# Optimization experiments

Measured on AMD Instinct MI355X. Metric: run time of the kernel, lower is better.

Reference implementation:

```python
import jax, jax.numpy as jnp
import numpy as np

NUM_EXPERTS = 8
HIDDEN = 1024
INTER = 1024
TOKENS = 2048
TOPK = 2


def setup_inputs() -> dict:
    key = jax.random.key(0)
    ks = jax.random.split(key, 7)
    hidden_states = jax.random.normal(ks[0], (TOKENS, HIDDEN), dtype=jnp.float32)
    router_weights = jax.random.uniform(ks[1], (TOKENS, TOPK), dtype=jnp.float32)
    selected_experts = jax.random.randint(ks[2], (TOKENS, TOPK), 0, NUM_EXPERTS, dtype=jnp.int32)
    token_per_expert = jax.random.randint(ks[3], (NUM_EXPERTS,), 0, 512, dtype=jnp.int32)
    # torch Linear weight layout is [out, in]; chunked along out-dim into E experts.
    # gate/up: [E, INTER, HIDDEN]; down: [E, HIDDEN, INTER]
    scale_h = 1.0 / np.sqrt(HIDDEN)
    scale_i = 1.0 / np.sqrt(INTER)
    gate_w = jax.random.normal(ks[4], (NUM_EXPERTS, INTER, HIDDEN), dtype=jnp.float32) * scale_h
    up_w = jax.random.normal(ks[5], (NUM_EXPERTS, INTER, HIDDEN), dtype=jnp.float32) * scale_h
    down_w = jax.random.normal(ks[6], (NUM_EXPERTS, HIDDEN, INTER), dtype=jnp.float32) * scale_i
    return {
        "hidden_states": hidden_states,
        "router_weights": router_weights,
        "selected_experts": selected_experts,
        "token_per_expert": token_per_expert,
        "gate_w": gate_w,
        "up_w": up_w,
        "down_w": down_w,
    }


def reference(hidden_states, router_weights, selected_experts, token_per_expert, gate_w, up_w, down_w):
    # Math equivalent of permute -> grouped GEMM (gate/up SwiGLU, down) -> unpermute+weighted combine.
    # Each (token, k) pair is routed to expert selected_experts[t,k] and scaled by router_weights[t,k]
    # (cast to fp32 as in the original), then summed over k.
    # Grouped GEMM out = x @ W_e^T; we evaluate every expert densely over all tokens and
    # combine with a one-hot routing matrix (clean, fully vectorized reference).
    x = hidden_states  # [T, H]
    g = jnp.einsum('th,eih->eti', x, gate_w)          # [E, T, I]
    u = jnp.einsum('th,eih->eti', x, up_w)            # [E, T, I]
    h = jax.nn.silu(g) * u                            # [E, T, I]
    out_e = jnp.einsum('eti,ehi->eth', h, down_w)     # [E, T, H]
    # combine[t, e] = sum_k router_weights[t, k] * 1[selected_experts[t, k] == e]
    onehot = jax.nn.one_hot(selected_experts, NUM_EXPERTS, dtype=jnp.float32)  # [T, K, E]
    combine = jnp.einsum('tk,tke->te', router_weights.astype(jnp.float32), onehot)  # [T, E]
    y = jnp.einsum('te,eth->th', combine, out_e)      # [T, H]
    return y
```

## Files before the change

kernel.cpp:

```cpp
#include <hip/hip_runtime.h>

#define HID   1024
#define NEXP  8
#define NPAIR 4096
#define BMPAD 128
#define PERM_MAX (NPAIR + NEXP * BMPAD)
#define MT_MAX (PERM_MAX / 128)

typedef unsigned short u16;
typedef __attribute__((ext_vector_type(8))) short bf16x8;
typedef __attribute__((ext_vector_type(4))) float f32x4;
typedef __attribute__((ext_vector_type(4))) unsigned short us4;

static __device__ __forceinline__ u16 f2bf(float f) {
  union { float f; unsigned u; } v; v.f = f;
  unsigned u = v.u;
  unsigned r = (u + 0x7fffu + ((u >> 16) & 1u)) >> 16;
  return (u16)r;
}

static __device__ __forceinline__ void gload16(const void* g, void* l) {
  __builtin_amdgcn_global_load_lds(
      (const __attribute__((address_space(1))) unsigned int*)g,
      (__attribute__((address_space(3))) unsigned int*)l, 16, 0, 0);
}

static __device__ __forceinline__ f32x4 mfma_bf16(bf16x8 a, bf16x8 b, f32x4 c) {
  return __builtin_amdgcn_mfma_f32_16x16x32_bf16(a, b, c, 0, 0, 0);
}

__global__ __launch_bounds__(256) void k_prep(const float* __restrict__ x,
                                              u16* __restrict__ xb,
                                              float* __restrict__ out) {
  int i = blockIdx.x * 256 + threadIdx.x;
  int base = i * 8;
  f32x4 v0 = *(const f32x4*)(x + base);
  f32x4 v1 = *(const f32x4*)(x + base + 4);
  us4 a = { f2bf(v0[0]), f2bf(v0[1]), f2bf(v0[2]), f2bf(v0[3]) };
  us4 b = { f2bf(v1[0]), f2bf(v1[1]), f2bf(v1[2]), f2bf(v1[3]) };
  *(us4*)(xb + base)     = a;
  *(us4*)(xb + base + 4) = b;
  f32x4 z = {0.f, 0.f, 0.f, 0.f};
  *(f32x4*)(out + base)     = z;
  *(f32x4*)(out + base + 4) = z;
}

__global__ __launch_bounds__(256) void k_convw(const float* __restrict__ g,
                                               const float* __restrict__ u,
                                               const float* __restrict__ d,
                                               u16* __restrict__ gb,
                                               u16* __restrict__ ub,
                                               u16* __restrict__ db) {
  const long NTH = 3L << 20;
  for (long i = (long)blockIdx.x * 256 + threadIdx.x; i < NTH; i += (long)gridDim.x * 256) {
    int which = (int)(i >> 20);
    long off = (i & ((1L << 20) - 1)) * 8;
    const float* src = which == 0 ? g : (which == 1 ? u : d);
    u16* dst = which == 0 ? gb : (which == 1 ? ub : db);
    f32x4 v0 = *(const f32x4*)(src + off);
    f32x4 v1 = *(const f32x4*)(src + off + 4);
    us4 a = { f2bf(v0[0]), f2bf(v0[1]), f2bf(v0[2]), f2bf(v0[3]) };
    us4 b = { f2bf(v1[0]), f2bf(v1[1]), f2bf(v1[2]), f2bf(v1[3]) };
    *(us4*)(dst + off)     = a;
    *(us4*)(dst + off + 4) = b;
  }
}

__global__ __launch_bounds__(256) void k_route(const int* __restrict__ sel,
                                               int* __restrict__ hdr,
                                               int* __restrict__ perm) {
  __shared__ int cnt[NEXP];
  __shared__ int cur[NEXP];
  int tid = threadIdx.x;
  if (tid < NEXP) cnt[tid] = 0;
  __syncthreads();
  for (int p = tid; p < NPAIR; p += 256) atomicAdd(&cnt[sel[p]], 1);
  __syncthreads();
  if (tid == 0) {
    int acc = 0;
    for (int e = 0; e < NEXP; e++) {
      hdr[e] = acc;
      cur[e] = acc;
      acc += (cnt[e] + 127) & ~127;
    }
    hdr[NEXP] = acc;
  }
  __syncthreads();
  for (int i = tid; i < PERM_MAX; i += 256) perm[i] = -1;
  __syncthreads();
  for (int p = tid; p < NPAIR; p += 256) {
    int e = sel[p];
    int slot = atomicAdd(&cur[e], 1);
    perm[slot] = p;
  }
}

__global__ __launch_bounds__(256) void k_gateup(const u16* __restrict__ xb,
                                                const u16* __restrict__ gwb,
                                                const u16* __restrict__ uwb,
                                                const int* __restrict__ hdr,
                                                const int* __restrict__ perm,
                                                u16* __restrict__ hbuf) {
  __shared__ __align__(16) u16 lA[128 * 64];
  __shared__ __align__(16) u16 lBg[64 * 64];
  __shared__ __align__(16) u16 lBu[64 * 64];

  const int tid = threadIdx.x, lane = tid & 63, wv = tid >> 6;
  const int n0 = blockIdx.x * 64, m0 = blockIdx.y * 128;
  const int total = hdr[NEXP];
  if (m0 >= total) return;
  int e = 0;
  #pragma unroll
  for (int k = 1; k < NEXP; k++) if (m0 >= hdr[k]) e = k;

  const u16* srcA[4]; u16* dstA[4];
  #pragma unroll
  for (int j = 0; j < 4; j++) {
    int rt = wv * 32 + j * 8 + (lane >> 3);
    int p = perm[m0 + rt];
    int tok = (p < 0) ? 0 : (p >> 1);
    int sw = (lane & 7) ^ (rt & 7);
    srcA[j] = xb + (size_t)tok * HID + sw * 8;
    dstA[j] = &lA[(wv * 32 + j * 8) * 64];
  }
  const u16* srcG[2]; const u16* srcU[2]; int dstBo[2];
  const size_t eb = (size_t)e * (1 << 20);
  #pragma unroll
  for (int j = 0; j < 2; j++) {
    int rt = wv * 16 + j * 8 + (lane >> 3);
    int sw = (lane & 7) ^ (rt & 7);
    srcG[j] = gwb + eb + (size_t)(n0 + rt) * HID + sw * 8;
    srcU[j] = uwb + eb + (size_t)(n0 + rt) * HID + sw * 8;
    dstBo[j] = (wv * 16 + j * 8) * 64;
  }

  const int wm = wv >> 1, wn = wv & 1;
  const int fr = lane & 15, fq = lane >> 4;

  f32x4 accg[4][2], accu[4][2];
  #pragma unroll
  for (int a = 0; a < 4; a++)
    #pragma unroll
    for (int b = 0; b < 2; b++) {
      accg[a][b] = (f32x4){0.f, 0.f, 0.f, 0.f};
      accu[a][b] = (f32x4){0.f, 0.f, 0.f, 0.f};
    }

  for (int kk = 0; kk < HID / 64; kk++) {
    const int k0 = kk * 64;
    #pragma unroll
    for (int j = 0; j < 4; j++) gload16(srcA[j] + k0, dstA[j]);
    #pragma unroll
    for (int j = 0; j < 2; j++) {
      gload16(srcG[j] + k0, &lBg[dstBo[j]]);
      gload16(srcU[j] + k0, &lBu[dstBo[j]]);
    }
    __syncthreads();
    #pragma unroll
    for (int kk2 = 0; kk2 < 2; kk2++) {
      bf16x8 af[4], bg[2], bu[2];
      #pragma unroll
      for (int m2 = 0; m2 < 4; m2++) {
        int r = wm * 64 + m2 * 16 + fr, q = kk2 * 4 + fq;
        af[m2] = *(const bf16x8*)&lA[r * 64 + (q ^ (r & 7)) * 8];
      }
      #pragma unroll
      for (int n2 = 0; n2 < 2; n2++) {
        int r = wn * 32 + n2 * 16 + fr, q = kk2 * 4 + fq;
        bg[n2] = *(const bf16x8*)&lBg[r * 64 + (q ^ (r & 7)) * 8];
        bu[n2] = *(const bf16x8*)&lBu[r * 64 + (q ^ (r & 7)) * 8];
      }
      #pragma unroll
      for (int m2 = 0; m2 < 4; m2++)
        #pragma unroll
        for (int n2 = 0; n2 < 2; n2++) {
          accg[m2][n2] = mfma_bf16(af[m2], bg[n2], accg[m2][n2]);
          accu[m2][n2] = mfma_bf16(af[m2], bu[n2], accu[m2][n2]);
        }
    }
    __syncthreads();
  }

  #pragma unroll
  for (int m2 = 0; m2 < 4; m2++)
    #pragma unroll
    for (int n2 = 0; n2 < 2; n2++)
      #pragma unroll
      for (int q = 0; q < 4; q++) {
        int row = m0 + wm * 64 + m2 * 16 + fq * 4 + q;
        int col = n0 + wn * 32 + n2 * 16 + fr;
        float g = accg[m2][n2][q];
        float u = accu[m2][n2][q];
        float h = (g / (1.0f + __expf(-g))) * u;
        hbuf[(size_t)row * HID + col] = f2bf(h);
      }
}

__global__ __launch_bounds__(256) void k_down(const u16* __restrict__ hbuf,
                                              const u16* __restrict__ dwb,
                                              const int* __restrict__ hdr,
                                              const int* __restrict__ perm,
                                              const float* __restrict__ rw,
                                              float* __restrict__ out) {
  __shared__ __align__(16) u16 lA[128 * 64];
  __shared__ __align__(16) u16 lB[64 * 64];

  const int tid = threadIdx.x, lane = tid & 63, wv = tid >> 6;
  const int n0 = blockIdx.x * 64, m0 = blockIdx.y * 128;
  const int total = hdr[NEXP];
  if (m0 >= total) return;
  int e = 0;
  #pragma unroll
  for (int k = 1; k < NEXP; k++) if (m0 >= hdr[k]) e = k;

  const u16* srcA[4]; u16* dstA[4];
  #pragma unroll
  for (int j = 0; j < 4; j++) {
    int rt = wv * 32 + j * 8 + (lane >> 3);
    int sw = (lane & 7) ^ (rt & 7);
    srcA[j] = hbuf + (size_t)(m0 + rt) * HID + sw * 8;
    dstA[j] = &lA[(wv * 32 + j * 8) * 64];
  }
  const u16* srcB[2]; int dstBo[2];
  const size_t eb = (size_t)e * (1 << 20);
  #pragma unroll
  for (int j = 0; j < 2; j++) {
    int rt = wv * 16 + j * 8 + (lane >> 3);
    int sw = (lane & 7) ^ (rt & 7);
    srcB[j] = dwb + eb + (size_t)(n0 + rt) * HID + sw * 8;
    dstBo[j] = (wv * 16 + j * 8) * 64;
  }

  const int wm = wv >> 1, wn = wv & 1;
  const int fr = lane & 15, fq = lane >> 4;

  f32x4 acc[4][2];
  #pragma unroll
  for (int a = 0; a < 4; a++)
    #pragma unroll
    for (int b = 0; b < 2; b++) acc[a][b] = (f32x4){0.f, 0.f, 0.f, 0.f};

  for (int kk = 0; kk < HID / 64; kk++) {
    const int k0 = kk * 64;
    #pragma unroll
    for (int j = 0; j < 4; j++) gload16(srcA[j] + k0, dstA[j]);
    #pragma unroll
    for (int j = 0; j < 2; j++) gload16(srcB[j] + k0, &lB[dstBo[j]]);
    __syncthreads();
    #pragma unroll
    for (int kk2 = 0; kk2 < 2; kk2++) {
      bf16x8 af[4], bf[2];
      #pragma unroll
      for (int m2 = 0; m2 < 4; m2++) {
        int r = wm * 64 + m2 * 16 + fr, q = kk2 * 4 + fq;
        af[m2] = *(const bf16x8*)&lA[r * 64 + (q ^ (r & 7)) * 8];
      }
      #pragma unroll
      for (int n2 = 0; n2 < 2; n2++) {
        int r = wn * 32 + n2 * 16 + fr, q = kk2 * 4 + fq;
        bf[n2] = *(const bf16x8*)&lB[r * 64 + (q ^ (r & 7)) * 8];
      }
      #pragma unroll
      for (int m2 = 0; m2 < 4; m2++)
        #pragma unroll
        for (int n2 = 0; n2 < 2; n2++)
          acc[m2][n2] = mfma_bf16(af[m2], bf[n2], acc[m2][n2]);
    }
    __syncthreads();
  }

  #pragma unroll
  for (int m2 = 0; m2 < 4; m2++)
    #pragma unroll
    for (int q = 0; q < 4; q++) {
      int row = m0 + wm * 64 + m2 * 16 + fq * 4 + q;
      int p = perm[row];
      if (p < 0) continue;
      int t = p >> 1;
      float w = rw[p];
      #pragma unroll
      for (int n2 = 0; n2 < 2; n2++) {
        int col = n0 + wn * 32 + n2 * 16 + fr;
        atomicAdd(&out[(size_t)t * HID + col], acc[m2][n2][q] * w);
      }
    }
}

extern "C" void kernel_launch(void* const* d_in, const int* in_sizes, int n_in,
                              void* d_out, int out_size, void* d_ws, size_t ws_size,
                              hipStream_t stream) {
  const float* x   = (const float*)d_in[0];
  const float* rw  = (const float*)d_in[1];
  const int*   sel = (const int*)d_in[2];
  const float* gw  = (const float*)d_in[4];
  const float* uw  = (const float*)d_in[5];
  const float* dw  = (const float*)d_in[6];
  float* out = (float*)d_out;

  char* ws = (char*)d_ws;
  int*  hdr  = (int*)ws;
  int*  perm = (int*)(ws + 1024);
  u16*  xb   = (u16*)(ws + (1 << 16));
  u16*  gwb  = xb + (2 << 20);
  u16*  uwb  = gwb + (8 << 20);
  u16*  dwb  = uwb + (8 << 20);
  u16*  hbuf = dwb + (8 << 20);

  k_prep <<<dim3(1024), dim3(256), 0, stream>>>(x, xb, out);
  k_convw<<<dim3(4096), dim3(256), 0, stream>>>(gw, uw, dw, gwb, uwb, dwb);
  k_route<<<dim3(1),    dim3(256), 0, stream>>>(sel, hdr, perm);
  k_gateup<<<dim3(16, MT_MAX), dim3(256), 0, stream>>>(xb, gwb, uwb, hdr, perm, hbuf);
  k_down  <<<dim3(16, MT_MAX), dim3(256), 0, stream>>>(hbuf, dwb, hdr, perm, rw, out);
}
```

Baseline: 114.4 us.

## Fuse fp32-to-bf16 weight conversion into GEMM loads with double-buffered LDS

Drops the separate weight-conversion kernel. The gate/up and down GEMMs now read fp32 weights directly into registers, pack them to bf16 and write them into LDS themselves. LDS tiles are double-buffered so the next K-slice's loads overlap the current MFMA work. This removes a full read and write of 48MB of fp32 weights plus bf16 copies and one launch. The cost is that each weight tile is re-read and re-converted by every M-tile block (up to 40 per expert column), doubling fp32 weight bytes per block and adding register pressure and more LDS.

```diff
diff --git a/kernel.cpp b/kernel.cpp
--- a/kernel.cpp
+++ b/kernel.cpp
@@ -1,4 +1,5 @@
 #include <hip/hip_runtime.h>
+#include <hip/hip_bf16.h>
 
 #define HID   1024
 #define NEXP  8
@@ -11,12 +12,18 @@
 typedef __attribute__((ext_vector_type(8))) short bf16x8;
 typedef __attribute__((ext_vector_type(4))) float f32x4;
 typedef __attribute__((ext_vector_type(4))) unsigned short us4;
+typedef __attribute__((ext_vector_type(4))) unsigned int u32x4;
 
 static __device__ __forceinline__ u16 f2bf(float f) {
   union { float f; unsigned u; } v; v.f = f;
   unsigned u = v.u;
   unsigned r = (u + 0x7fffu + ((u >> 16) & 1u)) >> 16;
   return (u16)r;
+}
+
+static __device__ __forceinline__ unsigned pk2(float a, float b) {
+  __hip_bfloat162 h = __float22bfloat162_rn(make_float2(a, b));
+  union { __hip_bfloat162 h; unsigned u; } c; c.h = h; return c.u;
 }
 
 static __device__ __forceinline__ void gload16(const void* g, void* l) {
@@ -45,27 +52,6 @@
   *(f32x4*)(out + base + 4) = z;
 }
 
-__global__ __launch_bounds__(256) void k_convw(const float* __restrict__ g,
-                                               const float* __restrict__ u,
-                                               const float* __restrict__ d,
-                                               u16* __restrict__ gb,
-                                               u16* __restrict__ ub,
-                                               u16* __restrict__ db) {
-  const long NTH = 3L << 20;
-  for (long i = (long)blockIdx.x * 256 + threadIdx.x; i < NTH; i += (long)gridDim.x * 256) {
-    int which = (int)(i >> 20);
-    long off = (i & ((1L << 20) - 1)) * 8;
-    const float* src = which == 0 ? g : (which == 1 ? u : d);
-    u16* dst = which == 0 ? gb : (which == 1 ? ub : db);
-    f32x4 v0 = *(const f32x4*)(src + off);
-    f32x4 v1 = *(const f32x4*)(src + off + 4);
-    us4 a = { f2bf(v0[0]), f2bf(v0[1]), f2bf(v0[2]), f2bf(v0[3]) };
-    us4 b = { f2bf(v1[0]), f2bf(v1[1]), f2bf(v1[2]), f2bf(v1[3]) };
-    *(us4*)(dst + off)     = a;
-    *(us4*)(dst + off + 4) = b;
-  }
-}
-
 __global__ __launch_bounds__(256) void k_route(const int* __restrict__ sel,
                                                int* __restrict__ hdr,
                                                int* __restrict__ perm) {
@@ -96,24 +82,23 @@
 }
 
 __global__ __launch_bounds__(256) void k_gateup(const u16* __restrict__ xb,
-                                                const u16* __restrict__ gwb,
-                                                const u16* __restrict__ uwb,
+                                                const float* __restrict__ gw,
+                                                const float* __restrict__ uw,
                                                 const int* __restrict__ hdr,
                                                 const int* __restrict__ perm,
                                                 u16* __restrict__ hbuf) {
-  __shared__ __align__(16) u16 lA[128 * 64];
-  __shared__ __align__(16) u16 lBg[64 * 64];
-  __shared__ __align__(16) u16 lBu[64 * 64];
+  __shared__ __align__(16) u16 lA[2][128 * 64];
+  __shared__ __align__(16) u16 lBg[2][64 * 64];
+  __shared__ __align__(16) u16 lBu[2][64 * 64];
 
   const int tid = threadIdx.x, lane = tid & 63, wv = tid >> 6;
   const int n0 = blockIdx.x * 64, m0 = blockIdx.y * 128;
-  const int total = hdr[NEXP];
-  if (m0 >= total) return;
+  if (m0 >= hdr[NEXP]) return;
   int e = 0;
   #pragma unroll
   for (int k = 1; k < NEXP; k++) if (m0 >= hdr[k]) e = k;
 
-  const u16* srcA[4]; u16* dstA[4];
+  const u16* srcA[4]; int dstAo[4];
   #pragma unroll
   for (int j = 0; j < 4; j++) {
     int rt = wv * 32 + j * 8 + (lane >> 3);
@@ -121,22 +106,20 @@
     int tok = (p < 0) ? 0 : (p >> 1);
     int sw = (lane & 7) ^ (rt & 7);
     srcA[j] = xb + (size_t)tok * HID + sw * 8;
-    dstA[j] = &lA[(wv * 32 + j * 8) * 64];
-  }
-  const u16* srcG[2]; const u16* srcU[2]; int dstBo[2];
+    dstAo[j] = (wv * 32 + j * 8) * 64;
+  }
+  const int br = wv * 16 + (lane >> 2);
+  const int cb = (lane & 3) * 16;
   const size_t eb = (size_t)e * (1 << 20);
-  #pragma unroll
-  for (int j = 0; j < 2; j++) {
-    int rt = wv * 16 + j * 8 + (lane >> 3);
-    int sw = (lane & 7) ^ (rt & 7);
-    srcG[j] = gwb + eb + (size_t)(n0 + rt) * HID + sw * 8;
-    srcU[j] = uwb + eb + (size_t)(n0 + rt) * HID + sw * 8;
-    dstBo[j] = (wv * 16 + j * 8) * 64;
-  }
+  const float* pG = gw + eb + (size_t)(n0 + br) * HID + cb;
+  const float* pU = uw + eb + (size_t)(n0 + br) * HID + cb;
+  const int bws0 = br * 64 + ((((lane & 3) * 2 + 0) ^ (br & 7)) * 8);
+  const int bws1 = br * 64 + ((((lane & 3) * 2 + 1) ^ (br & 7)) * 8);
 
   const int wm = wv >> 1, wn = wv & 1;
   const int fr = lane & 15, fq = lane >> 4;
 
+  f32x4 vg[4], vu[4];
   f32x4 accg[4][2], accu[4][2];
   #pragma unroll
   for (int a = 0; a < 4; a++)
@@ -146,40 +129,63 @@
       accu[a][b] = (f32x4){0.f, 0.f, 0.f, 0.f};
     }
 
-  for (int kk = 0; kk < HID / 64; kk++) {
-    const int k0 = kk * 64;
-    #pragma unroll
-    for (int j = 0; j < 4; j++) gload16(srcA[j] + k0, dstA[j]);
-    #pragma unroll
-    for (int j = 0; j < 2; j++) {
-      gload16(srcG[j] + k0, &lBg[dstBo[j]]);
-      gload16(srcU[j] + k0, &lBu[dstBo[j]]);
-    }
+#define GU_ISSUE(B, K0) { const int k0_ = (K0);                                   \
+    _Pragma("unroll") for (int j = 0; j < 4; j++)                                 \
+      gload16(srcA[j] + k0_, &lA[B][dstAo[j]]);                                   \
+    _Pragma("unroll") for (int i = 0; i < 4; i++) {                               \
+      vg[i] = *(const f32x4*)(pG + k0_ + i * 4);                                  \
+      vu[i] = *(const f32x4*)(pU + k0_ + i * 4);                                  \
+    } }
+
+#define GU_CVTW(B) {                                                              \
+    u32x4 w0 = { pk2(vg[0][0], vg[0][1]), pk2(vg[0][2], vg[0][3]),                \
+                 pk2(vg[1][0], vg[1][1]), pk2(vg[1][2], vg[1][3]) };              \
+    *(u32x4*)&lBg[B][bws0] = w0;                                                  \
+    u32x4 w1 = { pk2(vg[2][0], vg[2][1]), pk2(vg[2][2], vg[2][3]),                \
+                 pk2(vg[3][0], vg[3][1]), pk2(vg[3][2], vg[3][3]) };              \
+    *(u32x4*)&lBg[B][bws1] = w1;                                                  \
+    u32x4 w2 = { pk2(vu[0][0], vu[0][1]), pk2(vu[0][2], vu[0][3]),                \
+                 pk2(vu[1][0], vu[1][1]), pk2(vu[1][2], vu[1][3]) };              \
+    *(u32x4*)&lBu[B][bws0] = w2;                                                  \
+    u32x4 w3 = { pk2(vu[2][0], vu[2][1]), pk2(vu[2][2], vu[2][3]),                \
+                 pk2(vu[3][0], vu[3][1]), pk2(vu[3][2], vu[3][3]) };              \
+    *(u32x4*)&lBu[B][bws1] = w3; }
+
+#define GU_COMP(B) {                                                              \
+    _Pragma("unroll") for (int kk2 = 0; kk2 < 2; kk2++) {                         \
+      bf16x8 af[4], bg[2], bu[2];                                                 \
+      _Pragma("unroll") for (int m2 = 0; m2 < 4; m2++) {                          \
+        int r = wm * 64 + m2 * 16 + fr, q = kk2 * 4 + fq;                         \
+        af[m2] = *(const bf16x8*)&lA[B][r * 64 + (q ^ (r & 7)) * 8];              \
+      }                                                                           \
+      _Pragma("unroll") for (int n2 = 0; n2 < 2; n2++) {                          \
+        int r = wn * 32 + n2 * 16 + fr, q = kk2 * 4 + fq;                         \
+        bg[n2] = *(const bf16x8*)&lBg[B][r * 64 + (q ^ (r & 7)) * 8];             \
+        bu[n2] = *(const bf16x8*)&lBu[B][r * 64 + (q ^ (r & 7)) * 8];             \
+      }                                                                           \
+      _Pragma("unroll") for (int m2 = 0; m2 < 4; m2++)                            \
+        _Pragma("unroll") for (int n2 = 0; n2 < 2; n2++) {                        \
+          accg[m2][n2] = mfma_bf16(af[m2], bg[n2], accg[m2][n2]);                 \
+          accu[m2][n2] = mfma_bf16(af[m2], bu[n2], accu[m2][n2]);                 \
+        }                                                                         \
+    } }
+
+  GU_ISSUE(0, 0);
+  GU_CVTW(0);
+  __syncthreads();
+  for (int kk = 0; kk < 16; kk += 2) {
+    GU_ISSUE(1, (kk + 1) * 64);
+    GU_COMP(0);
+    GU_CVTW(1);
     __syncthreads();
-    #pragma unroll
-    for (int kk2 = 0; kk2 < 2; kk2++) {
-      bf16x8 af[4], bg[2], bu[2];
-      #pragma unroll
-      for (int m2 = 0; m2 < 4; m2++) {
-        int r = wm * 64 + m2 * 16 + fr, q = kk2 * 4 + fq;
-        af[m2] = *(const bf16x8*)&lA[r * 64 + (q ^ (r & 7)) * 8];
-      }
-      #pragma unroll
-      for (int n2 = 0; n2 < 2; n2++) {
-        int r = wn * 32 + n2 * 16 + fr, q = kk2 * 4 + fq;
-        bg[n2] = *(const bf16x8*)&lBg[r * 64 + (q ^ (r & 7)) * 8];
-        bu[n2] = *(const bf16x8*)&lBu[r * 64 + (q ^ (r & 7)) * 8];
-      }
-      #pragma unroll
-      for (int m2 = 0; m2 < 4; m2++)
-        #pragma unroll
-        for (int n2 = 0; n2 < 2; n2++) {
-          accg[m2][n2] = mfma_bf16(af[m2], bg[n2], accg[m2][n2]);
-          accu[m2][n2] = mfma_bf16(af[m2], bu[n2], accu[m2][n2]);
-        }
-    }
+    if (kk + 2 < 16) { GU_ISSUE(0, (kk + 2) * 64); }
+    GU_COMP(1);
+    if (kk + 2 < 16) { GU_CVTW(0); }
     __syncthreads();
   }
+#undef GU_ISSUE
+#undef GU_CVTW
+#undef GU_COMP
 
   #pragma unroll
   for (int m2 = 0; m2 < 4; m2++)
@@ -197,77 +203,92 @@
 }
 
 __global__ __launch_bounds__(256) void k_down(const u16* __restrict__ hbuf,
-                                              const u16* __restrict__ dwb,
+                                              const float* __restrict__ dw,
                                               const int* __restrict__ hdr,
                                               const int* __restrict__ perm,
                                               const float* __restrict__ rw,
                                               float* __restrict__ out) {
-  __shared__ __align__(16) u16 lA[128 * 64];
-  __shared__ __align__(16) u16 lB[64 * 64];
+  __shared__ __align__(16) u16 lA[2][128 * 64];
+  __shared__ __align__(16) u16 lB[2][64 * 64];
 
   const int tid = threadIdx.x, lane = tid & 63, wv = tid >> 6;
   const int n0 = blockIdx.x * 64, m0 = blockIdx.y * 128;
-  const int total = hdr[NEXP];
-  if (m0 >= total) return;
+  if (m0 >= hdr[NEXP]) return;
   int e = 0;
   #pragma unroll
   for (int k = 1; k < NEXP; k++) if (m0 >= hdr[k]) e = k;
 
-  const u16* srcA[4]; u16* dstA[4];
+  const u16* srcA[4]; int dstAo[4];
   #pragma unroll
   for (int j = 0; j < 4; j++) {
     int rt = wv * 32 + j * 8 + (lane >> 3);
     int sw = (lane & 7) ^ (rt & 7);
     srcA[j] = hbuf + (size_t)(m0 + rt) * HID + sw * 8;
-    dstA[j] = &lA[(wv * 32 + j * 8) * 64];
-  }
-  const u16* srcB[2]; int dstBo[2];
+    dstAo[j] = (wv * 32 + j * 8) * 64;
+  }
+  const int br = wv * 16 + (lane >> 2);
+  const int cb = (lane & 3) * 16;
   const size_t eb = (size_t)e * (1 << 20);
-  #pragma unroll
-  for (int j = 0; j < 2; j++) {
-    int rt = wv * 16 + j * 8 + (lane >> 3);
-    int sw = (lane & 7) ^ (rt & 7);
-    srcB[j] = dwb + eb + (size_t)(n0 + rt) * HID + sw * 8;
-    dstBo[j] = (wv * 16 + j * 8) * 64;
-  }
+  const float* pB = dw + eb + (size_t)(n0 + br) * HID + cb;
+  const int bws0 = br * 64 + ((((lane & 3) * 2 + 0) ^ (br & 7)) * 8);
+  const int bws1 = br * 64 + ((((lane & 3) * 2 + 1) ^ (br & 7)) * 8);
 
   const int wm = wv >> 1, wn = wv & 1;
   const int fr = lane & 15, fq = lane >> 4;
 
+  f32x4 vb[4];
   f32x4 acc[4][2];
   #pragma unroll
   for (int a = 0; a < 4; a++)
     #pragma unroll
     for (int b = 0; b < 2; b++) acc[a][b] = (f32x4){0.f, 0.f, 0.f, 0.f};
 
-  for (int kk = 0; kk < HID / 64; kk++) {
-    const int k0 = kk * 64;
-    #pragma unroll
-    for (int j = 0; j < 4; j++) gload16(srcA[j] + k0, dstA[j]);
-    #pragma unroll
-    for (int j = 0; j < 2; j++) gload16(srcB[j] + k0, &lB[dstBo[j]]);
+#define DN_ISSUE(B, K0) { const int k0_ = (K0);                                   \
+    _Pragma("unroll") for (int j = 0; j < 4; j++)                                 \
+      gload16(srcA[j] + k0_, &lA[B][dstAo[j]]);                                   \
+    _Pragma("unroll") for (int i = 0; i < 4; i++)                                 \
+      vb[i] = *(const f32x4*)(pB + k0_ + i * 4); }
+
+#define DN_CVTW(B) {                                                              \
+    u32x4 w0 = { pk2(vb[0][0], vb[0][1]), pk2(vb[0][2], vb[0][3]),                \
+                 pk2(vb[1][0], vb[1][1]), pk2(vb[1][2], vb[1][3]) };              \
+    *(u32x4*)&lB[B][bws0] = w0;                                                   \
+    u32x4 w1 = { pk2(vb[2][0], vb[2][1]), pk2(vb[2][2], vb[2][3]),                \
+                 pk2(vb[3][0], vb[3][1]), pk2(vb[3][2], vb[3][3]) };              \
+    *(u32x4*)&lB[B][bws1] = w1; }
+
+#define DN_COMP(B) {                                                              \
+    _Pragma("unroll") for (int kk2 = 0; kk2 < 2; kk2++) {                         \
+      bf16x8 af[4], bf[2];                                                        \
+      _Pragma("unroll") for (int m2 = 0; m2 < 4; m2++) {                          \
+        int r = wm * 64 + m2 * 16 + fr, q = kk2 * 4 + fq;                         \
+        af[m2] = *(const bf16x8*)&lA[B][r * 64 + (q ^ (r & 7)) * 8];              \
+      }                                                                           \
+      _Pragma("unroll") for (int n2 = 0; n2 < 2; n2++) {                          \
+        int r = wn * 32 + n2 * 16 + fr, q = kk2 * 4 + fq;                         \
+        bf[n2] = *(const bf16x8*)&lB[B][r * 64 + (q ^ (r & 7)) * 8];              \
+      }                                                                           \
+      _Pragma("unroll") for (int m2 = 0; m2 < 4; m2++)                            \
+        _Pragma("unroll") for (int n2 = 0; n2 < 2; n2++)                          \
+          acc[m2][n2] = mfma_bf16(af[m2], bf[n2], acc[m2][n2]);                   \
+    } }
+
+  DN_ISSUE(0, 0);
+  DN_CVTW(0);
+  __syncthreads();
+  for (int kk = 0; kk < 16; kk += 2) {
+    DN_ISSUE(1, (kk + 1) * 64);
+    DN_COMP(0);
+    DN_CVTW(1);
     __syncthreads();
-    #pragma unroll
-    for (int kk2 = 0; kk2 < 2; kk2++) {
-      bf16x8 af[4], bf[2];
-      #pragma unroll
-      for (int m2 = 0; m2 < 4; m2++) {
-        int r = wm * 64 + m2 * 16 + fr, q = kk2 * 4 + fq;
-        af[m2] = *(const bf16x8*)&lA[r * 64 + (q ^ (r & 7)) * 8];
-      }
-      #pragma unroll
-      for (int n2 = 0; n2 < 2; n2++) {
-        int r = wn * 32 + n2 * 16 + fr, q = kk2 * 4 + fq;
-        bf[n2] = *(const bf16x8*)&lB[r * 64 + (q ^ (r & 7)) * 8];
-      }
-      #pragma unroll
-      for (int m2 = 0; m2 < 4; m2++)
-        #pragma unroll
-        for (int n2 = 0; n2 < 2; n2++)
-          acc[m2][n2] = mfma_bf16(af[m2], bf[n2], acc[m2][n2]);
-    }
+    if (kk + 2 < 16) { DN_ISSUE(0, (kk + 2) * 64); }
+    DN_COMP(1);
+    if (kk + 2 < 16) { DN_CVTW(0); }
     __syncthreads();
   }
+#undef DN_ISSUE
+#undef DN_CVTW
+#undef DN_COMP
 
   #pragma unroll
   for (int m2 = 0; m2 < 4; m2++)
@@ -301,14 +322,10 @@
   int*  hdr  = (int*)ws;
   int*  perm = (int*)(ws + 1024);
   u16*  xb   = (u16*)(ws + (1 << 16));
-  u16*  gwb  = xb + (2 << 20);
-  u16*  uwb  = gwb + (8 << 20);
-  u16*  dwb  = uwb + (8 << 20);
-  u16*  hbuf = dwb + (8 << 20);
+  u16*  hbuf = xb + (2 << 20);
 
   k_prep <<<dim3(1024), dim3(256), 0, stream>>>(x, xb, out);
-  k_convw<<<dim3(4096), dim3(256), 0, stream>>>(gw, uw, dw, gwb, uwb, dwb);
   k_route<<<dim3(1),    dim3(256), 0, stream>>>(sel, hdr, perm);
-  k_gateup<<<dim3(16, MT_MAX), dim3(256), 0, stream>>>(xb, gwb, uwb, hdr, perm, hbuf);
-  k_down  <<<dim3(16, MT_MAX), dim3(256), 0, stream>>>(hbuf, dwb, hdr, perm, rw, out);
-}
+  k_gateup<<<dim3(16, MT_MAX), dim3(256), 0, stream>>>(xb, gw, uw, hdr, perm, hbuf);
+  k_down  <<<dim3(16, MT_MAX), dim3(256), 0, stream>>>(hbuf, dw, hdr, perm, rw, out);
+}
```

Measured after the change: 115.3 us. No clear change (+0.8%).

## Fuse weight conversion into prep and gate-up kernels, use per-expert grids

Applied to the files above, without the earlier changes.

Gate/up weight conversion moves into the prep kernel, and the down-weight conversion is folded into the tail of the gate-up kernel, which removes the separate conversion launch. Both GEMM kernels now use a 1D grid indexed by expert, N tile and M tile, and loop over M tiles in strides of 16. This avoids launching blocks that exit early on padded M tiles. The gate-up N tile shrinks to 32 to get more blocks. The trade-offs are narrower gate-up tiles with less B-tile reuse per A load, and extra conversion work in the gate-up tail.

```diff
diff --git a/kernel.cpp b/kernel.cpp
--- a/kernel.cpp
+++ b/kernel.cpp
@@ -1,11 +1,11 @@
 #include <hip/hip_runtime.h>
+#include <hip/hip_bf16.h>
 
 #define HID   1024
 #define NEXP  8
 #define NPAIR 4096
-#define BMPAD 128
-#define PERM_MAX (NPAIR + NEXP * BMPAD)
-#define MT_MAX (PERM_MAX / 128)
+#define PERM_MAX (NPAIR + NEXP * 128)
+#define MT_CAP 16
 
 typedef unsigned short u16;
 typedef __attribute__((ext_vector_type(8))) short bf16x8;
@@ -29,40 +29,36 @@
   return __builtin_amdgcn_mfma_f32_16x16x32_bf16(a, b, c, 0, 0, 0);
 }
 
-__global__ __launch_bounds__(256) void k_prep(const float* __restrict__ x,
-                                              u16* __restrict__ xb,
-                                              float* __restrict__ out) {
-  int i = blockIdx.x * 256 + threadIdx.x;
-  int base = i * 8;
-  f32x4 v0 = *(const f32x4*)(x + base);
-  f32x4 v1 = *(const f32x4*)(x + base + 4);
+static __device__ __forceinline__ void conv8(const float* src, u16* dst) {
+  f32x4 v0 = *(const f32x4*)src;
+  f32x4 v1 = *(const f32x4*)(src + 4);
   us4 a = { f2bf(v0[0]), f2bf(v0[1]), f2bf(v0[2]), f2bf(v0[3]) };
   us4 b = { f2bf(v1[0]), f2bf(v1[1]), f2bf(v1[2]), f2bf(v1[3]) };
-  *(us4*)(xb + base)     = a;
-  *(us4*)(xb + base + 4) = b;
-  f32x4 z = {0.f, 0.f, 0.f, 0.f};
-  *(f32x4*)(out + base)     = z;
-  *(f32x4*)(out + base + 4) = z;
-}
-
-__global__ __launch_bounds__(256) void k_convw(const float* __restrict__ g,
-                                               const float* __restrict__ u,
-                                               const float* __restrict__ d,
-                                               u16* __restrict__ gb,
-                                               u16* __restrict__ ub,
-                                               u16* __restrict__ db) {
-  const long NTH = 3L << 20;
-  for (long i = (long)blockIdx.x * 256 + threadIdx.x; i < NTH; i += (long)gridDim.x * 256) {
-    int which = (int)(i >> 20);
-    long off = (i & ((1L << 20) - 1)) * 8;
-    const float* src = which == 0 ? g : (which == 1 ? u : d);
-    u16* dst = which == 0 ? gb : (which == 1 ? ub : db);
-    f32x4 v0 = *(const f32x4*)(src + off);
-    f32x4 v1 = *(const f32x4*)(src + off + 4);
-    us4 a = { f2bf(v0[0]), f2bf(v0[1]), f2bf(v0[2]), f2bf(v0[3]) };
-    us4 b = { f2bf(v1[0]), f2bf(v1[1]), f2bf(v1[2]), f2bf(v1[3]) };
-    *(us4*)(dst + off)     = a;
-    *(us4*)(dst + off + 4) = b;
+  *(us4*)dst       = a;
+  *(us4*)(dst + 4) = b;
+}
+
+__global__ __launch_bounds__(256) void k_prep(const float* __restrict__ x,
+                                              const float* __restrict__ gw,
+                                              const float* __restrict__ uw,
+                                              u16* __restrict__ xb,
+                                              u16* __restrict__ gwb,
+                                              u16* __restrict__ uwb,
+                                              float* __restrict__ out) {
+  const int i = blockIdx.x * 256 + threadIdx.x;
+  {
+    int base = i * 8;
+    conv8(x + base, xb + base);
+    f32x4 z = {0.f, 0.f, 0.f, 0.f};
+    *(f32x4*)(out + base)     = z;
+    *(f32x4*)(out + base + 4) = z;
+  }
+  #pragma unroll
+  for (int j = 0; j < 4; j++) {
+    long c = (long)i + 262144L * j;
+    long off = c * 8;
+    conv8(gw + off, gwb + off);
+    conv8(uw + off, uwb + off);
   }
 }
 
@@ -98,102 +94,100 @@
 __global__ __launch_bounds__(256) void k_gateup(const u16* __restrict__ xb,
                                                 const u16* __restrict__ gwb,
                                                 const u16* __restrict__ uwb,
+                                                const float* __restrict__ dw,
+                                                u16* __restrict__ dwb,
                                                 const int* __restrict__ hdr,
                                                 const int* __restrict__ perm,
                                                 u16* __restrict__ hbuf) {
   __shared__ __align__(16) u16 lA[128 * 64];
-  __shared__ __align__(16) u16 lBg[64 * 64];
-  __shared__ __align__(16) u16 lBu[64 * 64];
+  __shared__ __align__(16) u16 lBg[32 * 64];
+  __shared__ __align__(16) u16 lBu[32 * 64];
 
   const int tid = threadIdx.x, lane = tid & 63, wv = tid >> 6;
-  const int n0 = blockIdx.x * 64, m0 = blockIdx.y * 128;
-  const int total = hdr[NEXP];
-  if (m0 >= total) return;
-  int e = 0;
-  #pragma unroll
-  for (int k = 1; k < NEXP; k++) if (m0 >= hdr[k]) e = k;
-
-  const u16* srcA[4]; u16* dstA[4];
-  #pragma unroll
-  for (int j = 0; j < 4; j++) {
-    int rt = wv * 32 + j * 8 + (lane >> 3);
-    int p = perm[m0 + rt];
-    int tok = (p < 0) ? 0 : (p >> 1);
-    int sw = (lane & 7) ^ (rt & 7);
-    srcA[j] = xb + (size_t)tok * HID + sw * 8;
-    dstA[j] = &lA[(wv * 32 + j * 8) * 64];
-  }
-  const u16* srcG[2]; const u16* srcU[2]; int dstBo[2];
-  const size_t eb = (size_t)e * (1 << 20);
-  #pragma unroll
-  for (int j = 0; j < 2; j++) {
-    int rt = wv * 16 + j * 8 + (lane >> 3);
-    int sw = (lane & 7) ^ (rt & 7);
-    srcG[j] = gwb + eb + (size_t)(n0 + rt) * HID + sw * 8;
-    srcU[j] = uwb + eb + (size_t)(n0 + rt) * HID + sw * 8;
-    dstBo[j] = (wv * 16 + j * 8) * 64;
-  }
+  const int bid = blockIdx.x;
+  const int e = bid & 7;
+  const int idx = bid >> 3;
+  const int nt = idx >> 4;
+  const int mt0 = idx & 15;
+  const int seg0 = hdr[e];
+  const int mcnt = (hdr[e + 1] - seg0) >> 7;
+  const int n0 = nt * 32;
 
   const int wm = wv >> 1, wn = wv & 1;
   const int fr = lane & 15, fq = lane >> 4;
-
-  f32x4 accg[4][2], accu[4][2];
-  #pragma unroll
-  for (int a = 0; a < 4; a++)
-    #pragma unroll
-    for (int b = 0; b < 2; b++) {
-      accg[a][b] = (f32x4){0.f, 0.f, 0.f, 0.f};
-      accu[a][b] = (f32x4){0.f, 0.f, 0.f, 0.f};
-    }
-
-  for (int kk = 0; kk < HID / 64; kk++) {
-    const int k0 = kk * 64;
-    #pragma unroll
-    for (int j = 0; j < 4; j++) gload16(srcA[j] + k0, dstA[j]);
-    #pragma unroll
-    for (int j = 0; j < 2; j++) {
-      gload16(srcG[j] + k0, &lBg[dstBo[j]]);
-      gload16(srcU[j] + k0, &lBu[dstBo[j]]);
-    }
-    __syncthreads();
-    #pragma unroll
-    for (int kk2 = 0; kk2 < 2; kk2++) {
-      bf16x8 af[4], bg[2], bu[2];
-      #pragma unroll
-      for (int m2 = 0; m2 < 4; m2++) {
-        int r = wm * 64 + m2 * 16 + fr, q = kk2 * 4 + fq;
-        af[m2] = *(const bf16x8*)&lA[r * 64 + (q ^ (r & 7)) * 8];
+  const size_t eb = (size_t)e << 20;
+
+  const int br = tid >> 3, bq = tid & 7;
+  const u16* srcG = gwb + eb + (size_t)(n0 + br) * HID + (bq ^ (br & 7)) * 8;
+  const u16* srcU = uwb + eb + (size_t)(n0 + br) * HID + (bq ^ (br & 7)) * 8;
+  const int dstBo = br * 64 + bq * 8;
+
+  for (int mt = mt0; mt < mcnt; mt += MT_CAP) {
+    const int m0 = seg0 + mt * 128;
+    const u16* srcA[4]; int dstAo[4];
+    #pragma unroll
+    for (int j = 0; j < 4; j++) {
+      int c = tid + 256 * j;
+      int r = c >> 3, q = c & 7;
+      int p = perm[m0 + r];
+      int tok = (p < 0) ? 0 : (p >> 1);
+      srcA[j] = xb + (size_t)tok * HID + (q ^ (r & 7)) * 8;
+      dstAo[j] = r * 64 + q * 8;
+    }
+
+    f32x4 accg[4], accu[4];
+    #pragma unroll
+    for (int a = 0; a < 4; a++) {
+      accg[a] = (f32x4){0.f, 0.f, 0.f, 0.f};
+      accu[a] = (f32x4){0.f, 0.f, 0.f, 0.f};
+    }
+
+    for (int kk = 0; kk < 16; kk++) {
+      const int k0 = kk * 64;
+      #pragma unroll
+      for (int j = 0; j < 4; j++) gload16(srcA[j] + k0, &lA[dstAo[j]]);
+      gload16(srcG + k0, &lBg[dstBo]);
+      gload16(srcU + k0, &lBu[dstBo]);
+      __syncthreads();
+      #pragma unroll
+      for (int kk2 = 0; kk2 < 2; kk2++) {
+        bf16x8 af[4], bg, bu;
+        #pragma unroll
+        for (int m2 = 0; m2 < 4; m2++) {
+          int r = wm * 64 + m2 * 16 + fr, q = kk2 * 4 + fq;
+          af[m2] = *(const bf16x8*)&lA[r * 64 + (q ^ (r & 7)) * 8];
+        }
+        {
+          int r = wn * 16 + fr, q = kk2 * 4 + fq;
+          bg = *(const bf16x8*)&lBg[r * 64 + (q ^ (r & 7)) * 8];
+          bu = *(const bf16x8*)&lBu[r * 64 + (q ^ (r & 7)) * 8];
+        }
+        #pragma unroll
+        for (int m2 = 0; m2 < 4; m2++) {
+          accg[m2] = mfma_bf16(af[m2], bg, accg[m2]);
+          accu[m2] = mfma_bf16(af[m2], bu, accu[m2]);
+        }
       }
-      #pragma unroll
-      for (int n2 = 0; n2 < 2; n2++) {
-        int r = wn * 32 + n2 * 16 + fr, q = kk2 * 4 + fq;
-        bg[n2] = *(const bf16x8*)&lBg[r * 64 + (q ^ (r & 7)) * 8];
-        bu[n2] = *(const bf16x8*)&lBu[r * 64 + (q ^ (r & 7)) * 8];
-      }
-      #pragma unroll
-      for (int m2 = 0; m2 < 4; m2++)
-        #pragma unroll
-        for (int n2 = 0; n2 < 2; n2++) {
-          accg[m2][n2] = mfma_bf16(af[m2], bg[n2], accg[m2][n2]);
-          accu[m2][n2] = mfma_bf16(af[m2], bu[n2], accu[m2][n2]);
-        }
-    }
-    __syncthreads();
-  }
-
-  #pragma unroll
-  for (int m2 = 0; m2 < 4; m2++)
-    #pragma unroll
-    for (int n2 = 0; n2 < 2; n2++)
+      __syncthreads();
+    }
+
+    #pragma unroll
+    for (int m2 = 0; m2 < 4; m2++)
       #pragma unroll
       for (int q = 0; q < 4; q++) {
         int row = m0 + wm * 64 + m2 * 16 + fq * 4 + q;
-        int col = n0 + wn * 32 + n2 * 16 + fr;
-        float g = accg[m2][n2][q];
-        float u = accu[m2][n2][q];
+        int col = n0 + wn * 16 + fr;
+        float g = accg[m2][q];
+        float u = accu[m2][q];
         float h = (g / (1.0f + __expf(-g))) * u;
         hbuf[(size_t)row * HID + col] = f2bf(h);
       }
+  }
+
+  {
+    long off = ((long)e << 20) + ((long)(idx * 256 + tid)) * 8;
+    conv8(dw + off, dwb + off);
+  }
 }
 
 __global__ __launch_bounds__(256) void k_down(const u16* __restrict__ hbuf,
@@ -206,84 +200,90 @@
   __shared__ __align__(16) u16 lB[64 * 64];
 
   const int tid = threadIdx.x, lane = tid & 63, wv = tid >> 6;
-  const int n0 = blockIdx.x * 64, m0 = blockIdx.y * 128;
-  const int total = hdr[NEXP];
-  if (m0 >= total) return;
-  int e = 0;
-  #pragma unroll
-  for (int k = 1; k < NEXP; k++) if (m0 >= hdr[k]) e = k;
-
-  const u16* srcA[4]; u16* dstA[4];
-  #pragma unroll
-  for (int j = 0; j < 4; j++) {
-    int rt = wv * 32 + j * 8 + (lane >> 3);
-    int sw = (lane & 7) ^ (rt & 7);
-    srcA[j] = hbuf + (size_t)(m0 + rt) * HID + sw * 8;
-    dstA[j] = &lA[(wv * 32 + j * 8) * 64];
-  }
+  const int bid = blockIdx.x;
+  const int e = bid & 7;
+  const int idx = bid >> 3;
+  const int nt = idx >> 4;
+  const int mt0 = idx & 15;
+  const int seg0 = hdr[e];
+  const int mcnt = (hdr[e + 1] - seg0) >> 7;
+  const int n0 = nt * 64;
+
+  const int wm = wv >> 1, wn = wv & 1;
+  const int fr = lane & 15, fq = lane >> 4;
+  const size_t eb = (size_t)e << 20;
+
   const u16* srcB[2]; int dstBo[2];
-  const size_t eb = (size_t)e * (1 << 20);
   #pragma unroll
   for (int j = 0; j < 2; j++) {
-    int rt = wv * 16 + j * 8 + (lane >> 3);
-    int sw = (lane & 7) ^ (rt & 7);
-    srcB[j] = dwb + eb + (size_t)(n0 + rt) * HID + sw * 8;
-    dstBo[j] = (wv * 16 + j * 8) * 64;
-  }
-
-  const int wm = wv >> 1, wn = wv & 1;
-  const int fr = lane & 15, fq = lane >> 4;
-
-  f32x4 acc[4][2];
-  #pragma unroll
-  for (int a = 0; a < 4; a++)
-    #pragma unroll
-    for (int b = 0; b < 2; b++) acc[a][b] = (f32x4){0.f, 0.f, 0.f, 0.f};
-
-  for (int kk = 0; kk < HID / 64; kk++) {
-    const int k0 = kk * 64;
-    #pragma unroll
-    for (int j = 0; j < 4; j++) gload16(srcA[j] + k0, dstA[j]);
-    #pragma unroll
-    for (int j = 0; j < 2; j++) gload16(srcB[j] + k0, &lB[dstBo[j]]);
-    __syncthreads();
-    #pragma unroll
-    for (int kk2 = 0; kk2 < 2; kk2++) {
-      bf16x8 af[4], bf[2];
-      #pragma unroll
-      for (int m2 = 0; m2 < 4; m2++) {
-        int r = wm * 64 + m2 * 16 + fr, q = kk2 * 4 + fq;
-        af[m2] = *(const bf16x8*)&lA[r * 64 + (q ^ (r & 7)) * 8];
+    int c = tid + 256 * j;
+    int r = c >> 3, q = c & 7;
+    srcB[j] = dwb + eb + (size_t)(n0 + r) * HID + (q ^ (r & 7)) * 8;
+    dstBo[j] = r * 64 + q * 8;
+  }
+
+  for (int mt = mt0; mt < mcnt; mt += MT_CAP) {
+    const int m0 = seg0 + mt * 128;
+    const u16* srcA[4]; int dstAo[4];
+    #pragma unroll
+    for (int j = 0; j < 4; j++) {
+      int c = tid + 256 * j;
+      int r = c >> 3, q = c & 7;
+      srcA[j] = hbuf + (size_t)(m0 + r) * HID + (q ^ (r & 7)) * 8;
+      dstAo[j] = r * 64 + q * 8;
+    }
+
+    f32x4 acc[4][2];
+    #pragma unroll
+    for (int a = 0; a < 4; a++)
+      #pragma unroll
+      for (int b = 0; b < 2; b++) acc[a][b] = (f32x4){0.f, 0.f, 0.f, 0.f};
+
+    for (int kk = 0; kk < 16; kk++) {
+      const int k0 = kk * 64;
+      #pragma unroll
+      for (int j = 0; j < 4; j++) gload16(srcA[j] + k0, &lA[dstAo[j]]);
+      #pragma unroll
+      for (int j = 0; j < 2; j++) gload16(srcB[j] + k0, &lB[dstBo[j]]);
+      __syncthreads();
+      #pragma unroll
+      for (int kk2 = 0; kk2 < 2; kk2++) {
+        bf16x8 af[4], bf[2];
+        #pragma unroll
+        for (int m2 = 0; m2 < 4; m2++) {
+          int r = wm * 64 + m2 * 16 + fr, q = kk2 * 4 + fq;
+          af[m2] = *(const bf16x8*)&lA[r * 64 + (q ^ (r & 7)) * 8];
+        }
+        #pragma unroll
+        for (int n2 = 0; n2 < 2; n2++) {
+          int r = wn * 32 + n2 * 16 + fr, q = kk2 * 4 + fq;
+          bf[n2] = *(const bf16x8*)&lB[r * 64 + (q ^ (r & 7)) * 8];
+        }
+        #pragma unroll
+        for (int m2 = 0; m2 < 4; m2++)
+          #pragma unroll
+          for (int n2 = 0; n2 < 2; n2++)
+            acc[m2][n2] = mfma_bf16(af[m2], bf[n2], acc[m2][n2]);
       }
-      #pragma unroll
-      for (int n2 = 0; n2 < 2; n2++) {
-        int r = wn * 32 + n2 * 16 + fr, q = kk2 * 4 + fq;
-        bf[n2] = *(const bf16x8*)&lB[r * 64 + (q ^ (r & 7)) * 8];
+      __syncthreads();
+    }
+
+    #pragma unroll
+    for (int m2 = 0; m2 < 4; m2++)
+      #pragma unroll
+      for (int q = 0; q < 4; q++) {
+        int row = m0 + wm * 64 + m2 * 16 + fq * 4 + q;
+        int p = perm[row];
+        if (p < 0) continue;
+        int t = p >> 1;
+        float w = rw[p];
+        #pragma unroll
+        for (int n2 = 0; n2 < 2; n2++) {
+          int col = n0 + wn * 32 + n2 * 16 + fr;
+          atomicAdd(&out[(size_t)t * HID + col], acc[m2][n2][q] * w);
+        }
       }
-      #pragma unroll
-      for (int m2 = 0; m2 < 4; m2++)
-        #pragma unroll
-        for (int n2 = 0; n2 < 2; n2++)
-          acc[m2][n2] = mfma_bf16(af[m2], bf[n2], acc[m2][n2]);
-    }
-    __syncthreads();
-  }
-
-  #pragma unroll
-  for (int m2 = 0; m2 < 4; m2++)
-    #pragma unroll
-    for (int q = 0; q < 4; q++) {
-      int row = m0 + wm * 64 + m2 * 16 + fq * 4 + q;
-      int p = perm[row];
-      if (p < 0) continue;
-      int t = p >> 1;
-      float w = rw[p];
-      #pragma unroll
-      for (int n2 = 0; n2 < 2; n2++) {
-        int col = n0 + wn * 32 + n2 * 16 + fr;
-        atomicAdd(&out[(size_t)t * HID + col], acc[m2][n2][q] * w);
-      }
-    }
+  }
 }
 
 extern "C" void kernel_launch(void* const* d_in, const int* in_sizes, int n_in,
@@ -306,9 +306,8 @@
   u16*  dwb  = uwb + (8 << 20);
   u16*  hbuf = dwb + (8 << 20);
 
-  k_prep <<<dim3(1024), dim3(256), 0, stream>>>(x, xb, out);
-  k_convw<<<dim3(4096), dim3(256), 0, stream>>>(gw, uw, dw, gwb, uwb, dwb);
-  k_route<<<dim3(1),    dim3(256), 0, stream>>>(sel, hdr, perm);
-  k_gateup<<<dim3(16, MT_MAX), dim3(256), 0, stream>>>(xb, gwb, uwb, hdr, perm, hbuf);
-  k_down  <<<dim3(16, MT_MAX), dim3(256), 0, stream>>>(hbuf, dwb, hdr, perm, rw, out);
-}
+  k_prep  <<<dim3(1024), dim3(256), 0, stream>>>(x, gw, uw, xb, gwb, uwb, out);
+  k_route <<<dim3(1),    dim3(256), 0, stream>>>(sel, hdr, perm);
+  k_gateup<<<dim3(8 * 32 * MT_CAP), dim3(256), 0, stream>>>(xb, gwb, uwb, dw, dwb, hdr, perm, hbuf);
+  k_down  <<<dim3(8 * 16 * MT_CAP), dim3(256), 0, stream>>>(hbuf, dwb, hdr, perm, rw, out);
+}
```

Result: slower. 126.1 us (+10.3%).
